# Kernel optimization log

Hardware: AMD Instinct MI355X
Metric: run time of the kernel (lower is better)

The kernel has to match this reference:

```python
import jax, jax.numpy as jnp
import numpy as np

SCALING = 1.0


def setup_inputs() -> dict:
    key = jax.random.key(0)
    k1, k2, k3, k4, k5, k6 = jax.random.split(key, 6)
    in_f, out_f, r = 4096, 4096, 32
    nnz = r * (in_f + out_f)  # 262144
    x = jax.random.normal(k1, (4, 2048, in_f), dtype=jnp.float32)
    weight = jax.random.normal(k2, (out_f, in_f), dtype=jnp.float32) * 0.02
    bias = jax.random.normal(k3, (out_f,), dtype=jnp.float32) * 0.02
    shira_weight = jax.random.normal(k4, (nnz,), dtype=jnp.float32) * 0.02
    rows = jax.random.randint(k5, (1, nnz), 0, out_f, dtype=jnp.int32)
    cols = jax.random.randint(k6, (1, nnz), 0, in_f, dtype=jnp.int32)
    shira_indices = jnp.concatenate([rows, cols], axis=0)  # [2, nnz]
    return {"x": x, "weight": weight, "bias": bias,
            "shira_weight": shira_weight, "shira_indices": shira_indices}


def reference(x, weight, bias, shira_weight, shira_indices):
    # delta = sparse_coo(indices, shira_weight * scaling) densified into weight copy
    new_weight = weight.at[shira_indices[0], shira_indices[1]].add(shira_weight * SCALING)
    # F.linear: x @ W^T + b
    return jnp.einsum('bsi,oi->bso', x, new_weight) + bias
```

## Files before the change

kernel.cpp:

```cpp
#include <hip/hip_runtime.h>
#include <hip/hip_bf16.h>
#include <stdint.h>

typedef float v4f __attribute__((ext_vector_type(4)));
typedef short v8s __attribute__((ext_vector_type(8)));

#define GEMM_M 8192
#define GEMM_N 4096
#define GEMM_K 4096
#define BM 128
#define BN 128
#define BK 64


__device__ __forceinline__ uint16_t f2bf(float f) {
    union { float f; uint32_t u; } v; v.f = f;
    uint32_t r = v.u + 0x7FFFu + ((v.u >> 16) & 1u);
    return (uint16_t)(r >> 16);
}

__device__ __forceinline__ float bf2f(uint16_t h) {
    union { uint32_t u; float f; } v; v.u = ((uint32_t)h) << 16;
    return v.f;
}

__device__ __forceinline__ void cvt8(const float* __restrict__ s, uint16_t* __restrict__ d) {
    float4 a = ((const float4*)s)[0];
    float4 b = ((const float4*)s)[1];
    union { v8s v; uint16_t u[8]; } o;
    o.u[0] = f2bf(a.x); o.u[1] = f2bf(a.y); o.u[2] = f2bf(a.z); o.u[3] = f2bf(a.w);
    o.u[4] = f2bf(b.x); o.u[5] = f2bf(b.y); o.u[6] = f2bf(b.z); o.u[7] = f2bf(b.w);
    *(v8s*)d = o.v;
}

__global__ void prep_cvt_kernel(const float* __restrict__ X, const float* __restrict__ W,
                                uint16_t* __restrict__ Xb, uint16_t* __restrict__ Wb,
                                size_t x8) {
    size_t i = (size_t)blockIdx.x * blockDim.x + threadIdx.x;
    if (i < x8) {
        cvt8(X + i * 8, Xb + i * 8);
    } else {
        size_t j = i - x8;
        cvt8(W + j * 8, Wb + j * 8);
    }
}

__global__ void scatter_bf16_kernel(uint16_t* __restrict__ Wb, const float* __restrict__ vals,
                                    const int* __restrict__ rows, const int* __restrict__ cols,
                                    int nnz) {
    int i = blockIdx.x * blockDim.x + threadIdx.x;
    if (i >= nnz) return;
    size_t idx = (size_t)rows[i] * GEMM_K + cols[i];
    uint32_t* addr = (uint32_t*)Wb + (idx >> 1);
    const bool hi = idx & 1;
    const float v = vals[i];
    uint32_t cur = *addr, assumed;
    do {
        assumed = cur;
        uint16_t h = hi ? (uint16_t)(assumed >> 16) : (uint16_t)(assumed & 0xFFFFu);
        uint16_t nh = f2bf(bf2f(h) + v);
        uint32_t nw = hi ? ((assumed & 0x0000FFFFu) | ((uint32_t)nh << 16))
                         : ((assumed & 0xFFFF0000u) | (uint32_t)nh);
        if (nw == assumed) break;
        cur = atomicCAS(addr, assumed, nw);
    } while (cur != assumed);
}


__device__ __forceinline__ void gload_lds16(const void* g, void* lds) {
    __builtin_amdgcn_global_load_lds(
        (const __attribute__((address_space(1))) void*)(uintptr_t)g,
        (__attribute__((address_space(3))) void*)(uintptr_t)lds,
        16, 0, 0);
}

__global__ __launch_bounds__(256) void gemm_bt_kernel(
    const uint16_t* __restrict__ A,
    const uint16_t* __restrict__ B,
    const float* __restrict__ bias,
    float* __restrict__ C)
{
    __shared__ __attribute__((aligned(16))) uint16_t As[BM * BK];
    __shared__ __attribute__((aligned(16))) uint16_t Bs[BN * BK];

    const int tid  = threadIdx.x;
    const int lane = tid & 63;
    const int wv   = tid >> 6;
    const int wy   = wv >> 1;
    const int wx   = wv & 1;
    const int lrow = lane & 15;
    const int quad = lane >> 4;

    const int m0 = blockIdx.y * BM;
    const int n0 = blockIdx.x * BN;

    const int srow = wv * 32 + (lane >> 3);
    const int skc  = ((lane & 7) ^ (lane >> 3)) * 8;
    const uint16_t* a_g = A + (size_t)(m0 + srow) * GEMM_K + skc;
    const uint16_t* b_g = B + (size_t)(n0 + srow) * GEMM_K + skc;
    uint16_t* a_l = As + (size_t)(wv * 256 + lane) * 8;
    uint16_t* b_l = Bs + (size_t)(wv * 256 + lane) * 8;

    v4f acc[4][4];
#pragma unroll
    for (int i = 0; i < 4; i++)
#pragma unroll
        for (int j = 0; j < 4; j++) acc[i][j] = (v4f){0.f, 0.f, 0.f, 0.f};

    const int xr = lrow & 7;

    for (int k0 = 0; k0 < GEMM_K; k0 += BK) {
#pragma unroll
        for (int i = 0; i < 4; i++) {
            gload_lds16(a_g + k0 + (size_t)i * 8 * GEMM_K, a_l + i * 512);
            gload_lds16(b_g + k0 + (size_t)i * 8 * GEMM_K, b_l + i * 512);
        }
        __syncthreads();

#pragma unroll
        for (int h = 0; h < 2; h++) {
            v8s af[4], bf[4];
#pragma unroll
            for (int t = 0; t < 4; t++) {
                const int row = wy * 64 + t * 16 + lrow;
                af[t] = *(const v8s*)(As + row * BK + (((h * 4 + quad) ^ xr) * 8));
            }
#pragma unroll
            for (int t = 0; t < 4; t++) {
                const int row = wx * 64 + t * 16 + lrow;
                bf[t] = *(const v8s*)(Bs + row * BK + (((h * 4 + quad) ^ xr) * 8));
            }
#pragma unroll
            for (int i = 0; i < 4; i++)
#pragma unroll
                for (int j = 0; j < 4; j++)
                    acc[i][j] = __builtin_amdgcn_mfma_f32_16x16x32_bf16(af[i], bf[j], acc[i][j], 0, 0, 0);
        }

        __syncthreads();
    }

#pragma unroll
    for (int j = 0; j < 4; j++) {
        const int col = n0 + wx * 64 + j * 16 + lrow;
        const float bj = bias[col];
#pragma unroll
        for (int i = 0; i < 4; i++) {
            const int row = m0 + wy * 64 + i * 16 + quad * 4;
            float* cp = C + (size_t)row * GEMM_N + col;
#pragma unroll
            for (int r = 0; r < 4; r++)
                cp[(size_t)r * GEMM_N] = acc[i][j][r] + bj;
        }
    }
}


extern "C" void kernel_launch(void* const* d_in, const int* in_sizes, int n_in,
                              void* d_out, int out_size, void* d_ws, size_t ws_size,
                              hipStream_t stream) {
    const float* x      = (const float*)d_in[0];
    const float* weight = (const float*)d_in[1];
    const float* bias   = (const float*)d_in[2];
    const float* sw     = (const float*)d_in[3];
    const int*   sidx   = (const int*)d_in[4];
    const int nnz = in_sizes[3];

    const size_t welems = (size_t)GEMM_N * GEMM_K;
    const size_t xelems = (size_t)GEMM_M * GEMM_K;

    uint16_t* Wb = (uint16_t*)d_ws;
    uint16_t* Xb = (uint16_t*)((char*)d_ws + welems * sizeof(uint16_t));

    const size_t x8 = xelems / 8;
    const size_t w8 = welems / 8;
    const int prep_blocks = (int)((x8 + w8) / 256);

    prep_cvt_kernel<<<dim3(prep_blocks), 256, 0, stream>>>(x, weight, Xb, Wb, x8);
    scatter_bf16_kernel<<<dim3((nnz + 255) / 256), 256, 0, stream>>>(
        Wb, sw, sidx, sidx + nnz, nnz);
    gemm_bt_kernel<<<dim3(GEMM_N / BN, GEMM_M / BM), 256, 0, stream>>>(
        Xb, Wb, bias, (float*)d_out);
}
```

Before: 588.9 us.

## Rewrite GEMM as 256x256 tile, 8-wave, double-buffered pipelined kernel with block swizzle

Replaces the 128x128 single-buffered GEMM with a 256x256 tile handled by 512 threads. The tile is split into four 128x128 quadrants with double-buffered LDS and asynchronous global-to-LDS loads issued two k-steps ahead, interleaved with MFMA phases using explicit waitcnt, barriers and setprio. It also remaps block IDs for L2 locality. The aim is to hide memory latency and raise arithmetic intensity, at the cost of more registers, a larger LDS footprint and fragile hand-tuned synchronization.

Measured after the change: 503.1 us. 1.17x faster.

```diff
diff --git a/kernel.cpp b/kernel.cpp
--- a/kernel.cpp
+++ b/kernel.cpp
@@ -8,9 +8,10 @@
 #define GEMM_M 8192
 #define GEMM_N 4096
 #define GEMM_K 4096
-#define BM 128
-#define BN 128
+#define BM 256
+#define BN 256
 #define BK 64
+#define NT (GEMM_K / BK)
 
 
 __device__ __forceinline__ uint16_t f2bf(float f) {
@@ -74,85 +75,166 @@
         16, 0, 0);
 }
 
-__global__ __launch_bounds__(256) void gemm_bt_kernel(
+__global__ __launch_bounds__(512, 2) void gemm_bt_kernel(
     const uint16_t* __restrict__ A,
     const uint16_t* __restrict__ B,
     const float* __restrict__ bias,
     float* __restrict__ C)
 {
-    __shared__ __attribute__((aligned(16))) uint16_t As[BM * BK];
-    __shared__ __attribute__((aligned(16))) uint16_t Bs[BN * BK];
+    __shared__ __attribute__((aligned(16))) uint16_t As[2][2][128 * BK];
+    __shared__ __attribute__((aligned(16))) uint16_t Bs[2][2][128 * BK];
 
     const int tid  = threadIdx.x;
     const int lane = tid & 63;
-    const int wv   = tid >> 6;
-    const int wy   = wv >> 1;
-    const int wx   = wv & 1;
+    const int wid  = tid >> 6;
+    const int wm2  = wid >> 1;
+    const int wn2  = wid & 1;
     const int lrow = lane & 15;
     const int quad = lane >> 4;
-
-    const int m0 = blockIdx.y * BM;
-    const int n0 = blockIdx.x * BN;
-
-    const int srow = wv * 32 + (lane >> 3);
+    const int xr   = lane & 7;
+
+    const int bid = blockIdx.x;
+    const int swz = (bid & 7) * 64 + (bid >> 3);
+    const int m0  = (swz >> 4) * BM;
+    const int n0  = (swz & 15) * BN;
+
+    const int srow = wid * 16 + (lane >> 3);
     const int skc  = ((lane & 7) ^ (lane >> 3)) * 8;
-    const uint16_t* a_g = A + (size_t)(m0 + srow) * GEMM_K + skc;
-    const uint16_t* b_g = B + (size_t)(n0 + srow) * GEMM_K + skc;
-    uint16_t* a_l = As + (size_t)(wv * 256 + lane) * 8;
-    uint16_t* b_l = Bs + (size_t)(wv * 256 + lane) * 8;
-
-    v4f acc[4][4];
+    const uint16_t* gA = A + (size_t)(m0 + srow) * GEMM_K + skc;
+    const uint16_t* gB = B + (size_t)(n0 + srow) * GEMM_K + skc;
+    const int ldso = wid * 1024 + lane * 8;
+
+#define STAGE(gbase, hrow, s, ldshalf)  do {                                   \
+        const uint16_t* _g = (gbase) + (size_t)(hrow) * GEMM_K + (s) * BK;     \
+        uint16_t* _l = (ldshalf) + ldso;                                       \
+        gload_lds16(_g, _l);                                                   \
+        gload_lds16(_g + (size_t)8 * GEMM_K, _l + 512);                        \
+    } while (0)
+
+    v4f acc00[2][4], acc10[2][4], acc01[2][4], acc11[2][4];
 #pragma unroll
-    for (int i = 0; i < 4; i++)
+    for (int mi = 0; mi < 2; ++mi)
 #pragma unroll
-        for (int j = 0; j < 4; j++) acc[i][j] = (v4f){0.f, 0.f, 0.f, 0.f};
-
-    const int xr = lrow & 7;
-
-    for (int k0 = 0; k0 < GEMM_K; k0 += BK) {
-#pragma unroll
-        for (int i = 0; i < 4; i++) {
-            gload_lds16(a_g + k0 + (size_t)i * 8 * GEMM_K, a_l + i * 512);
-            gload_lds16(b_g + k0 + (size_t)i * 8 * GEMM_K, b_l + i * 512);
+        for (int nj = 0; nj < 4; ++nj) {
+            acc00[mi][nj] = (v4f){0.f, 0.f, 0.f, 0.f};
+            acc10[mi][nj] = (v4f){0.f, 0.f, 0.f, 0.f};
+            acc01[mi][nj] = (v4f){0.f, 0.f, 0.f, 0.f};
+            acc11[mi][nj] = (v4f){0.f, 0.f, 0.f, 0.f};
         }
-        __syncthreads();
-
-#pragma unroll
-        for (int h = 0; h < 2; h++) {
-            v8s af[4], bf[4];
-#pragma unroll
-            for (int t = 0; t < 4; t++) {
-                const int row = wy * 64 + t * 16 + lrow;
-                af[t] = *(const v8s*)(As + row * BK + (((h * 4 + quad) ^ xr) * 8));
-            }
-#pragma unroll
-            for (int t = 0; t < 4; t++) {
-                const int row = wx * 64 + t * 16 + lrow;
-                bf[t] = *(const v8s*)(Bs + row * BK + (((h * 4 + quad) ^ xr) * 8));
-            }
-#pragma unroll
-            for (int i = 0; i < 4; i++)
-#pragma unroll
-                for (int j = 0; j < 4; j++)
-                    acc[i][j] = __builtin_amdgcn_mfma_f32_16x16x32_bf16(af[i], bf[j], acc[i][j], 0, 0, 0);
-        }
-
-        __syncthreads();
+
+    v8s a0F[2][2], a1F[2][2], bF[4][2];
+
+#define LDA(dst, hp) do {                                                      \
+        _Pragma("unroll")                                                      \
+        for (int mi = 0; mi < 2; ++mi)                                         \
+        _Pragma("unroll")                                                      \
+        for (int ks = 0; ks < 2; ++ks) {                                       \
+            const int rh = wm2 * 32 + mi * 16 + lrow;                          \
+            const int c  = ks * 4 + quad;                                      \
+            dst[mi][ks] = *(const v8s*)((hp) + rh * BK + ((c ^ xr) << 3));     \
+        } } while (0)
+
+#define LDB(hp) do {                                                           \
+        _Pragma("unroll")                                                      \
+        for (int nj = 0; nj < 4; ++nj)                                         \
+        _Pragma("unroll")                                                      \
+        for (int ks = 0; ks < 2; ++ks) {                                       \
+            const int rh = wn2 * 64 + nj * 16 + lrow;                          \
+            const int c  = ks * 4 + quad;                                      \
+            bF[nj][ks] = *(const v8s*)((hp) + rh * BK + ((c ^ xr) << 3));      \
+        } } while (0)
+
+#define MM(accq, aT) do {                                                      \
+        _Pragma("unroll")                                                      \
+        for (int ks = 0; ks < 2; ++ks)                                         \
+        _Pragma("unroll")                                                      \
+        for (int mi = 0; mi < 2; ++mi)                                         \
+        _Pragma("unroll")                                                      \
+        for (int nj = 0; nj < 4; ++nj)                                         \
+            accq[mi][nj] = __builtin_amdgcn_mfma_f32_16x16x32_bf16(            \
+                aT[mi][ks], bF[nj][ks], accq[mi][nj], 0, 0, 0);                \
+    } while (0)
+
+#define BAR()   __builtin_amdgcn_s_barrier()
+#define LGKM0() asm volatile("s_waitcnt lgkmcnt(0)" ::: "memory")
+#define VM6()   asm volatile("s_waitcnt vmcnt(6)" ::: "memory")
+#define SCHED() __builtin_amdgcn_sched_barrier(0)
+
+    STAGE(gA, 0,   0, &As[0][0][0]);
+    STAGE(gA, 128, 0, &As[0][1][0]);
+    STAGE(gB, 0,   0, &Bs[0][0][0]);
+    STAGE(gB, 128, 0, &Bs[0][1][0]);
+    STAGE(gA, 0,   1, &As[1][0][0]);
+    STAGE(gA, 128, 1, &As[1][1][0]);
+    STAGE(gB, 0,   1, &Bs[1][0][0]);
+    SCHED(); VM6();
+    BAR();
+
+#define TILE(t, b) do {                                                        \
+        const int s1 = ((t) + 1) & (NT - 1);                                   \
+        const int s2 = ((t) + 2) & (NT - 1);                                   \
+                                                       \
+        LDA(a0F, &As[b][0][0]);                                                \
+        LDB(&Bs[b][0][0]);                                                     \
+        STAGE(gB, 128, s1, &Bs[(b) ^ 1][1][0]);                                \
+        SCHED(); BAR(); LGKM0(); SCHED();                                      \
+        __builtin_amdgcn_s_setprio(1); MM(acc00, a0F); __builtin_amdgcn_s_setprio(0); \
+        SCHED(); BAR();                                                        \
+                                                       \
+        LDA(a1F, &As[b][1][0]);                                                \
+        STAGE(gA, 0, s2, &As[b][0][0]);                                        \
+        SCHED(); BAR(); LGKM0(); SCHED();                                      \
+        __builtin_amdgcn_s_setprio(1); MM(acc10, a1F); __builtin_amdgcn_s_setprio(0); \
+        SCHED(); BAR();                                                        \
+                                                       \
+        LDB(&Bs[b][1][0]);                                                     \
+        STAGE(gA, 128, s2, &As[b][1][0]);                                      \
+        SCHED(); BAR(); LGKM0(); SCHED();                                      \
+        __builtin_amdgcn_s_setprio(1); MM(acc01, a0F); __builtin_amdgcn_s_setprio(0); \
+        SCHED(); BAR();                                                        \
+                 \
+        STAGE(gB, 0, s2, &Bs[b][0][0]);                                        \
+        SCHED(); VM6();                                                        \
+        BAR();                                                                 \
+        __builtin_amdgcn_s_setprio(1); MM(acc11, a1F); __builtin_amdgcn_s_setprio(0); \
+        SCHED(); BAR();                                                        \
+    } while (0)
+
+    for (int t = 0; t < NT; t += 2) {
+        TILE(t, 0);
+        TILE(t + 1, 1);
     }
 
-#pragma unroll
-    for (int j = 0; j < 4; j++) {
-        const int col = n0 + wx * 64 + j * 16 + lrow;
-        const float bj = bias[col];
-#pragma unroll
-        for (int i = 0; i < 4; i++) {
-            const int row = m0 + wy * 64 + i * 16 + quad * 4;
-            float* cp = C + (size_t)row * GEMM_N + col;
-#pragma unroll
-            for (int r = 0; r < 4; r++)
-                cp[(size_t)r * GEMM_N] = acc[i][j][r] + bj;
-        }
-    }
+#define WR(accq, QM, QN) do {                                                  \
+        _Pragma("unroll")                                                      \
+        for (int nj = 0; nj < 4; ++nj) {                                       \
+            const int col = n0 + (QN) * 128 + wn2 * 64 + nj * 16 + lrow;       \
+            const float bj = bias[col];                                        \
+            _Pragma("unroll")                                                  \
+            for (int mi = 0; mi < 2; ++mi) {                                   \
+                const int row = m0 + (QM) * 128 + wm2 * 32 + mi * 16 + quad * 4; \
+                float* cp = C + (size_t)row * GEMM_N + col;                    \
+                _Pragma("unroll")                                              \
+                for (int r = 0; r < 4; ++r)                                    \
+                    cp[(size_t)r * GEMM_N] = accq[mi][nj][r] + bj;             \
+            }                                                                  \
+        } } while (0)
+
+    WR(acc00, 0, 0);
+    WR(acc10, 1, 0);
+    WR(acc01, 0, 1);
+    WR(acc11, 1, 1);
+
+#undef STAGE
+#undef LDA
+#undef LDB
+#undef MM
+#undef BAR
+#undef LGKM0
+#undef VM6
+#undef SCHED
+#undef TILE
+#undef WR
 }
 
 
@@ -179,6 +261,6 @@
     prep_cvt_kernel<<<dim3(prep_blocks), 256, 0, stream>>>(x, weight, Xb, Wb, x8);
     scatter_bf16_kernel<<<dim3((nnz + 255) / 256), 256, 0, stream>>>(
         Wb, sw, sidx, sidx + nnz, nnz);
-    gemm_bt_kernel<<<dim3(GEMM_N / BN, GEMM_M / BM), 256, 0, stream>>>(
+    gemm_bt_kernel<<<dim3((GEMM_M / BM) * (GEMM_N / BN)), 512, 0, stream>>>(
         Xb, Wb, bias, (float*)d_out);
 }
```
